# Kernel tuning notes

Hardware: AMD Instinct MI355X
Metric: run time of the kernel (lower is better)

The kernel has to match this reference:

```python
import jax, jax.numpy as jnp
import numpy as np
import math

B, S, D, H = 4, 1024, 2048, 16
DH = D // H          # dim_head = 128
DHID = 128           # dim_hid
DKER = 64            # dim_ker
EPS = 1e-6


def setup_inputs() -> dict:
    key = jax.random.key(0)
    ks = jax.random.split(key, 12)
    a1 = math.sqrt(6.0 / (DH + DHID))
    a2 = math.sqrt(6.0 / (DKER + DHID))
    a3 = math.sqrt(6.0 / (2 * DKER))
    return {
        "q": jax.random.normal(ks[0], (B, S, D), jnp.float32),
        "k": jax.random.normal(ks[1], (B, S, D), jnp.float32),
        "v": jax.random.normal(ks[2], (B, S, D), jnp.float32),
        "lr_attn_mask": jax.random.randint(ks[3], (B, 1, S, S), 0, 2).astype(bool),
        "sparse_norms_lse": jax.random.normal(ks[4], (B, H, S, 1), jnp.float32),
        "sparse_attn_weights": jax.random.normal(ks[5], (B, H, S, S), jnp.float32),
        "kernel_q_mat1": jax.random.uniform(ks[6], (H, DH, DHID), jnp.float32, -a1, a1),
        "kernel_k_mat1": jax.random.uniform(ks[7], (H, DH, DHID), jnp.float32, -a1, a1),
        "kernel_q_mat2": jax.random.uniform(ks[8], (H, DHID, DKER), jnp.float32, -a2, a2),
        "kernel_k_mat2": jax.random.uniform(ks[9], (H, DHID, DKER), jnp.float32, -a2, a2),
        "interaction_k": jax.random.uniform(ks[10], (H, DKER, DKER), jnp.float32, -a3, a3),
        "scalingD": jnp.ones((1, H, 1, DKER), jnp.float32) * 1e-4,
        "scalingD2": jnp.ones((1, H, 1, DKER), jnp.float32) * 1e-4,
        "lambda_constant": 1,
    }


def _gelu(x):
    # torch F.gelu default = exact (erf) gelu
    return jax.nn.gelu(x, approximate=False)


def reference(q, k, v, lr_attn_mask, sparse_norms_lse, sparse_attn_weights,
              kernel_q_mat1, kernel_k_mat1, kernel_q_mat2, kernel_k_mat2,
              interaction_k, scalingD, scalingD2, lambda_constant):
    # split heads: [B,S,D] -> [B,H,S,DH]
    qh = q.reshape(B, S, H, DH).transpose(0, 2, 1, 3)
    kh = k.reshape(B, S, H, DH).transpose(0, 2, 1, 3)
    vh = v.reshape(B, S, H, DH).transpose(0, 2, 1, 3)

    # learned kernel feature maps (dropout=0 -> identity)
    qf = _gelu(jnp.einsum('bhsd,hde->bhse', qh, kernel_q_mat1))
    qf = _gelu(jnp.einsum('bhse,hef->bhsf', qf, kernel_q_mat2))

    kf = _gelu(jnp.einsum('bhsd,hde->bhse', kh, kernel_k_mat1))
    kf = jnp.abs(scalingD) * _gelu(jnp.einsum('bhse,hef->bhsf', kf, kernel_k_mat2))
    kf = kf + jnp.einsum('bhse,hef->bhsf', kf, interaction_k) * scalingD2

    # low-rank (kernelized) scores, masked. [B,H,S,S]
    scores = jnp.einsum('bhse,bhte->bhst', jnp.abs(qf), jnp.abs(kf))
    m = lr_attn_mask.astype(scores.dtype)  # [B,1,S,S] broadcasts
    scores = m * scores

    # log-domain merge with external sparse attention
    lr_norms_lse = jnp.log(scores.sum(axis=-1, keepdims=True) + EPS)
    norm_factor_lse = jnp.logaddexp(lr_norms_lse, sparse_norms_lse)
    logits = jnp.log(scores + EPS) * m + (1.0 - m) * sparse_attn_weights
    attn = jnp.exp(logits - norm_factor_lse)

    out = jnp.einsum('bhst,bhtd->bhsd', attn, vh)
    return out.transpose(0, 2, 1, 3).reshape(B, S, D)
```

## Files before the change

kernel.cpp:

```cpp
#include <hip/hip_runtime.h>


typedef __bf16 bf16_t;
typedef __attribute__((ext_vector_type(8))) __bf16 bf16x8;
typedef __attribute__((ext_vector_type(4))) float f32x4;

#define MFMA(a, b, c) __builtin_amdgcn_mfma_f32_16x16x32_bf16((a), (b), (c), 0, 0, 0)

typedef __attribute__((address_space(3))) void as3_void;
typedef __attribute__((address_space(1))) const void as1_void;
static __device__ __forceinline__ void gload16(const void* g, void* l) {
    __builtin_amdgcn_global_load_lds((as1_void*)g, (as3_void*)l, 16, 0, 0);
}

static __device__ __forceinline__ float gelu_exact(float x) {
    return 0.5f * x * (1.0f + erff(x * 0.70710678118654752f));
}

static __device__ __forceinline__ unsigned pack_bf16(float a, float b) {
    bf16_t x = (bf16_t)a, y = (bf16_t)b;
    unsigned short ux = __builtin_bit_cast(unsigned short, x);
    unsigned short uy = __builtin_bit_cast(unsigned short, y);
    return (unsigned)ux | ((unsigned)uy << 16);
}

__global__ __launch_bounds__(256) void conv_weights_kernel(
    const float* __restrict__ wq1, const float* __restrict__ wk1,
    const float* __restrict__ wq2, const float* __restrict__ wk2,
    const float* __restrict__ iK,
    bf16_t* __restrict__ wq1t, bf16_t* __restrict__ wk1t,
    bf16_t* __restrict__ wq2t, bf16_t* __restrict__ wk2t,
    bf16_t* __restrict__ iKt)
{
    const int idx = blockIdx.x * 256 + threadIdx.x;
    if (idx < 16 * 128 * 128) {
        int h = idx >> 14, e = (idx >> 7) & 127, d = idx & 127;
        wq1t[idx] = (bf16_t)wq1[(h << 14) + (d << 7) + e];
        wk1t[idx] = (bf16_t)wk1[(h << 14) + (d << 7) + e];
    }
    if (idx < 16 * 64 * 128) {
        int h = idx >> 13, f = (idx >> 7) & 63, e = idx & 127;
        wq2t[idx] = (bf16_t)wq2[(h << 13) + (e << 6) + f];
        wk2t[idx] = (bf16_t)wk2[(h << 13) + (e << 6) + f];
    }
    if (idx < 16 * 64 * 64) {
        int h = idx >> 12, g = (idx >> 6) & 63, f = idx & 63;
        iKt[idx] = (bf16_t)iK[(h << 12) + (f << 6) + g];
    }
}

__global__ __launch_bounds__(256) void prep_kernel(
    const float* __restrict__ q, const float* __restrict__ k,
    const float* __restrict__ v, const unsigned char* __restrict__ mask8,
    const bf16_t* __restrict__ wq1t, const bf16_t* __restrict__ wq2t,
    const bf16_t* __restrict__ wk1t, const bf16_t* __restrict__ wk2t,
    const bf16_t* __restrict__ iKt,
    const float* __restrict__ sD, const float* __restrict__ sD2,
    bf16_t* __restrict__ qf, bf16_t* __restrict__ kf,
    bf16_t* __restrict__ vT, unsigned char* __restrict__ mprep)
{
    __shared__ char smem[44032];
    const int bxg = blockIdx.x;
    const int tid = threadIdx.x;

    if (bxg < 1024) {
        __shared__ int mflag;
        if (tid == 0) {
            unsigned a = 0;
            for (int i = 0; i < 64; ++i) a |= mask8[4 * i + 1];
            mflag = (a == 0) ? 1 : 0;
        }
        __syncthreads();
        const size_t base = ((size_t)bxg * 256 + tid) * 16;
        if (mflag) {
            const int* mi = (const int*)mask8;
            uint4 r;
            unsigned bs[4];
#pragma unroll
            for (int j = 0; j < 4; ++j) {
                int4 vv = *reinterpret_cast<const int4*>(&mi[base + j * 4]);
                bs[j] = (vv.x ? 1u : 0u) | ((vv.y ? 1u : 0u) << 8) |
                        ((vv.z ? 1u : 0u) << 16) | ((vv.w ? 1u : 0u) << 24);
            }
            r.x = bs[0]; r.y = bs[1]; r.z = bs[2]; r.w = bs[3];
            *reinterpret_cast<uint4*>(&mprep[base]) = r;
        } else {
            uint4 vv = *reinterpret_cast<const uint4*>(&mask8[base]);
            uint4 r;
            unsigned* pv = (unsigned*)&vv;
            unsigned* pr = (unsigned*)&r;
#pragma unroll
            for (int j = 0; j < 4; ++j) {
                unsigned x = pv[j], o = 0;
#pragma unroll
                for (int kk = 0; kk < 4; ++kk)
                    o |= (((x >> (8 * kk)) & 255u) ? 1u : 0u) << (8 * kk);
                pr[j] = o;
            }
            *reinterpret_cast<uint4*>(&mprep[base]) = r;
        }
        return;
    }

    if (bxg < 2048) {
        typedef bf16_t tr_t[72];
        tr_t* tr = reinterpret_cast<tr_t*>(smem);
        const int idv = bxg - 1024;
        const int bh = idv & 63, b = bh >> 4, h = bh & 15;
        const int tt = idv >> 6;
        const int t0 = tt * 64;
#pragma unroll
        for (int i = 0; i < 8; ++i) {
            int f4 = tid + 256 * i;
            int t = f4 >> 5, c4 = f4 & 31;
            const float4 vv = *reinterpret_cast<const float4*>(
                &v[((size_t)b * 1024 + t0 + t) * 2048 + h * 128 + c4 * 4]);
            tr[c4 * 4 + 0][t] = (bf16_t)vv.x;
            tr[c4 * 4 + 1][t] = (bf16_t)vv.y;
            tr[c4 * 4 + 2][t] = (bf16_t)vv.z;
            tr[c4 * 4 + 3][t] = (bf16_t)vv.w;
        }
        __syncthreads();
#pragma unroll
        for (int i = 0; i < 32; ++i) {
            int e = tid + 256 * i;
            int d = e >> 6, tl = e & 63;
            vT[(((size_t)bh * 16 + tt) * 128 + d) * 64 + tl] = tr[d][tl];
        }
        return;
    }

    {
        typedef bf16_t row136[136];
        typedef bf16_t row72[72];
        row136* xa = reinterpret_cast<row136*>(smem);
        row136* h1 = reinterpret_cast<row136*>(smem + 17408);
        row72*  k2 = reinterpret_cast<row72*>(smem + 34816);

        const int idf = bxg - 2048;
        const int lane = tid & 63, w = tid >> 6;
        const int lr = lane & 15, lg = lane >> 4;
        const int row0 = (idf & 63) * 64;
        const int h = (idf >> 6) & 15;
        const int path = idf >> 10;

        const float* X = path ? k : q;
        const bf16_t* w1t = path ? wk1t : wq1t;
        const bf16_t* w2t = path ? wk2t : wq2t;
        bf16_t* outp = path ? kf : qf;

#pragma unroll
        for (int i = 0; i < 8; ++i) {
            int f4 = tid + 256 * i;
            int r = f4 >> 5, c4 = f4 & 31;
            const float4 vv = *reinterpret_cast<const float4*>(
                &X[(size_t)(row0 + r) * 2048 + h * 128 + c4 * 4]);
            xa[r][c4 * 4 + 0] = (bf16_t)vv.x;
            xa[r][c4 * 4 + 1] = (bf16_t)vv.y;
            xa[r][c4 * 4 + 2] = (bf16_t)vv.z;
            xa[r][c4 * 4 + 3] = (bf16_t)vv.w;
        }
        __syncthreads();

        bf16x8 a1[4];
#pragma unroll
        for (int kk = 0; kk < 4; ++kk)
            a1[kk] = *reinterpret_cast<const bf16x8*>(&xa[w * 16 + lr][kk * 32 + lg * 8]);
#pragma unroll
        for (int nt = 0; nt < 8; ++nt) {
            f32x4 acc = {0.f, 0.f, 0.f, 0.f};
#pragma unroll
            for (int kk = 0; kk < 4; ++kk) {
                bf16x8 bfr = *reinterpret_cast<const bf16x8*>(
                    &w1t[(size_t)h * 16384 + (nt * 16 + lr) * 128 + kk * 32 + lg * 8]);
                acc = MFMA(a1[kk], bfr, acc);
            }
#pragma unroll
            for (int r = 0; r < 4; ++r)
                h1[w * 16 + lg * 4 + r][nt * 16 + lr] = (bf16_t)gelu_exact(acc[r]);
        }
        __syncthreads();

        bf16x8 a2[4];
#pragma unroll
        for (int kk = 0; kk < 4; ++kk)
            a2[kk] = *reinterpret_cast<const bf16x8*>(&h1[w * 16 + lr][kk * 32 + lg * 8]);

        if (path == 0) {
#pragma unroll
            for (int nt = 0; nt < 4; ++nt) {
                f32x4 acc = {0.f, 0.f, 0.f, 0.f};
#pragma unroll
                for (int kk = 0; kk < 4; ++kk) {
                    bf16x8 bfr = *reinterpret_cast<const bf16x8*>(
                        &w2t[(size_t)h * 8192 + (nt * 16 + lr) * 128 + kk * 32 + lg * 8]);
                    acc = MFMA(a2[kk], bfr, acc);
                }
#pragma unroll
                for (int r = 0; r < 4; ++r) {
                    int n = row0 + w * 16 + lg * 4 + r;
                    int bb = n >> 10, s = n & 1023;
                    outp[(((size_t)bb * 16 + h) * 1024 + s) * 64 + nt * 16 + lr] =
                        (bf16_t)fabsf(gelu_exact(acc[r]));
                }
            }
        } else {
#pragma unroll
            for (int nt = 0; nt < 4; ++nt) {
                f32x4 acc = {0.f, 0.f, 0.f, 0.f};
#pragma unroll
                for (int kk = 0; kk < 4; ++kk) {
                    bf16x8 bfr = *reinterpret_cast<const bf16x8*>(
                        &w2t[(size_t)h * 8192 + (nt * 16 + lr) * 128 + kk * 32 + lg * 8]);
                    acc = MFMA(a2[kk], bfr, acc);
                }
#pragma unroll
                for (int r = 0; r < 4; ++r) {
                    int f = nt * 16 + lr;
                    k2[w * 16 + lg * 4 + r][f] =
                        (bf16_t)(fabsf(sD[h * 64 + f]) * gelu_exact(acc[r]));
                }
            }
            __syncthreads();
            bf16x8 a3[2];
#pragma unroll
            for (int kk = 0; kk < 2; ++kk)
                a3[kk] = *reinterpret_cast<const bf16x8*>(&k2[w * 16 + lr][kk * 32 + lg * 8]);
#pragma unroll
            for (int nt = 0; nt < 4; ++nt) {
                f32x4 acc = {0.f, 0.f, 0.f, 0.f};
#pragma unroll
                for (int kk = 0; kk < 2; ++kk) {
                    bf16x8 bfr = *reinterpret_cast<const bf16x8*>(
                        &iKt[(size_t)h * 4096 + (nt * 16 + lr) * 64 + kk * 32 + lg * 8]);
                    acc = MFMA(a3[kk], bfr, acc);
                }
#pragma unroll
                for (int r = 0; r < 4; ++r) {
                    int row = w * 16 + lg * 4 + r;
                    int g = nt * 16 + lr;
                    float base = (float)k2[row][g];
                    float kv = fabsf(base + acc[r] * sD2[h * 64 + g]);
                    int n = row0 + row;
                    int bb = n >> 10, s = n & 1023;
                    outp[(((size_t)bb * 16 + h) * 1024 + s) * 64 + g] = (bf16_t)kv;
                }
            }
        }
    }
}

__global__ __launch_bounds__(256, 2) void attn_cv_kernel(
    const bf16_t* __restrict__ qf, const bf16_t* __restrict__ kf,
    const bf16_t* __restrict__ vT,
    const unsigned char* __restrict__ mprep,
    const float* __restrict__ saw, const float* __restrict__ lse,
    float* __restrict__ out)
{
    __shared__ bf16_t vbuf[3][128 * 64];
    __shared__ bf16_t kbuf[3][64 * 64];

    const int tid = threadIdx.x;
    const int lane = tid & 63, w = tid >> 6;
    const int lr = lane & 15, lg = lane >> 4;

    const int di = blockIdx.y * 16 + blockIdx.x;
    const int xcd = di & 7, rr = di >> 3;
    const int bh = xcd + 8 * (rr >> 4);
    const int s0 = (rr & 15) * 64;
    const int b = bh >> 4, h = bh & 15;

    const int srow = s0 + w * 16 + lr;
    const size_t saw_row = ((size_t)bh << 20) + (size_t)srow * 1024;
    const size_t m_row   = ((size_t)b << 20) + (size_t)srow * 1024;

    const int vrow = tid >> 3;
    const int vcol8 = (tid & 7) ^ (vrow & 7);
    const bf16_t* vt_bh = vT + (size_t)bh * 131072;
    const bf16_t* kf_bh = kf + (size_t)bh * 65536;

    bf16x8 aq0, aq1;
    {
        const size_t qb = ((size_t)bh * 1024 + srow) * 64;
        aq0 = *reinterpret_cast<const bf16x8*>(&qf[qb + lg * 8]);
        aq1 = *reinterpret_cast<const bf16x8*>(&qf[qb + 32 + lg * 8]);
    }

    const f32x4 fzero = {0.f, 0.f, 0.f, 0.f};
    f32x4 oacc[8];
#pragma unroll
    for (int i = 0; i < 8; ++i) oacc[i] = fzero;
    float rs = 0.f;

#define STAGE_VT(BUF, TILE)                                                      \
    {                                                                            \
        const bf16_t* vg = vt_bh + (size_t)(TILE) * 8192 + vcol8 * 8;            \
        char* lb = (char*)&vbuf[BUF][0] + w * 1024;                              \
        _Pragma("unroll")                                                        \
        for (int j = 0; j < 4; ++j)                                              \
            gload16(vg + (size_t)(32 * j + vrow) * 64, lb + j * 4096);           \
    }

#define STAGE_KF(BUF, TILE)                                                      \
    {                                                                            \
        const bf16_t* kg = kf_bh + (size_t)(TILE) * 4096 + vcol8 * 8;            \
        char* lb = (char*)&kbuf[BUF][0] + w * 1024;                              \
        _Pragma("unroll")                                                        \
        for (int j = 0; j < 2; ++j)                                              \
            gload16(kg + (size_t)(32 * j + vrow) * 64, lb + j * 4096);           \
    }

#define LOAD_SAW(TILE, SS, MM)                                                   \
    {                                                                            \
        _Pragma("unroll")                                                        \
        for (int nt = 0; nt < 4; ++nt) {                                         \
            SS[nt] = *reinterpret_cast<const f32x4*>(                            \
                &saw[saw_row + (size_t)(TILE) * 64 + nt * 16 + lg * 4]);         \
            MM[nt] = *reinterpret_cast<const unsigned*>(                         \
                &mprep[m_row + (size_t)(TILE) * 64 + nt * 16 + lg * 4]);         \
        }                                                                        \
    }

#define QKT_MERGE(CUR, SS, MM)                                                   \
    {                                                                            \
        _Pragma("unroll")                                                        \
        for (int nt = 0; nt < 4; ++nt) {                                         \
            const int row = nt * 16 + lr;                                        \
            const char* kb = (const char*)&kbuf[CUR][0] + row * 128;             \
            const int sw = (row & 7) * 16;                                       \
            bf16x8 k0 = *reinterpret_cast<const bf16x8*>(kb + ((lg * 16) ^ sw)); \
            bf16x8 k1 = *reinterpret_cast<const bf16x8*>(kb + ((64 + lg * 16) ^ sw)); \
            f32x4 acc = fzero;                                                   \
            acc = MFMA(k0, aq0, acc);                                            \
            acc = MFMA(k1, aq1, acc);                                            \
            const unsigned mm = MM[nt];                                          \
            float v0, v1, v2, v3;                                                \
            v0 = (mm & 255u)         ? (acc[0] + 1e-6f) : __expf(SS[nt][0]);     \
            rs += (mm & 255u)         ? acc[0] : 0.f;                            \
            v1 = ((mm >> 8) & 255u)  ? (acc[1] + 1e-6f) : __expf(SS[nt][1]);     \
            rs += ((mm >> 8) & 255u)  ? acc[1] : 0.f;                            \
            v2 = ((mm >> 16) & 255u) ? (acc[2] + 1e-6f) : __expf(SS[nt][2]);     \
            rs += ((mm >> 16) & 255u) ? acc[2] : 0.f;                            \
            v3 = (mm >> 24)          ? (acc[3] + 1e-6f) : __expf(SS[nt][3]);     \
            rs += (mm >> 24)          ? acc[3] : 0.f;                            \
            pk[nt * 2]     = pack_bf16(v0, v1);                                  \
            pk[nt * 2 + 1] = pack_bf16(v2, v3);                                  \
        }                                                                        \
    }

#define REDIST()                                                                 \
    {                                                                            \
        const int srcA = lr + ((lg & 1) << 5);                                   \
        const int srcB = srcA + 16;                                              \
        const bool sel = (lg < 2);                                               \
        const unsigned a0 = __shfl(pk[0], srcA, 64);                             \
        const unsigned a1 = __shfl(pk[1], srcA, 64);                             \
        const unsigned a2 = __shfl(pk[2], srcA, 64);                             \
        const unsigned a3 = __shfl(pk[3], srcA, 64);                             \
        const unsigned b0 = __shfl(pk[0], srcB, 64);                             \
        const unsigned b1 = __shfl(pk[1], srcB, 64);                             \
        const unsigned b2 = __shfl(pk[2], srcB, 64);                             \
        const unsigned b3 = __shfl(pk[3], srcB, 64);                             \
        f0w.x = sel ? a0 : a2;  f0w.y = sel ? a1 : a3;                           \
        f0w.z = sel ? b0 : b2;  f0w.w = sel ? b1 : b3;                           \
        const unsigned c4 = __shfl(pk[4], srcA, 64);                             \
        const unsigned c5 = __shfl(pk[5], srcA, 64);                             \
        const unsigned c6 = __shfl(pk[6], srcA, 64);                             \
        const unsigned c7 = __shfl(pk[7], srcA, 64);                             \
        const unsigned d4 = __shfl(pk[4], srcB, 64);                             \
        const unsigned d5 = __shfl(pk[5], srcB, 64);                             \
        const unsigned d6 = __shfl(pk[6], srcB, 64);                             \
        const unsigned d7 = __shfl(pk[7], srcB, 64);                             \
        f1w.x = sel ? c4 : c6;  f1w.y = sel ? c5 : c7;                           \
        f1w.z = sel ? d4 : d6;  f1w.w = sel ? d5 : d7;                           \
    }

#define PV(CUR)                                                                  \
    {                                                                            \
        bf16x8 pf0 = __builtin_bit_cast(bf16x8, f0w);                            \
        bf16x8 pf1 = __builtin_bit_cast(bf16x8, f1w);                            \
        __builtin_amdgcn_s_setprio(1);                                           \
        _Pragma("unroll")                                                        \
        for (int dt = 0; dt < 8; ++dt) {                                         \
            const int row = dt * 16 + lr;                                        \
            const char* vb = (const char*)&vbuf[CUR][0] + row * 128;             \
            const int sw = (row & 7) * 16;                                       \
            bf16x8 v0 = *reinterpret_cast<const bf16x8*>(vb + ((lg * 16) ^ sw)); \
            bf16x8 v1 = *reinterpret_cast<const bf16x8*>(vb + ((64 + lg * 16) ^ sw)); \
            oacc[dt] = MFMA(v0, pf0, oacc[dt]);                                  \
            oacc[dt] = MFMA(v1, pf1, oacc[dt]);                                  \
        }                                                                        \
        __builtin_amdgcn_s_setprio(0);                                           \
    }

#define FULL_PHASE(CIDX, SIDX, TSTAGE, SS, MM, TSAW)                             \
    {                                                                            \
        STAGE_VT(SIDX, TSTAGE);                                                  \
        STAGE_KF(SIDX, TSTAGE);                                                  \
        __builtin_amdgcn_sched_barrier(0);                                       \
        asm volatile("s_waitcnt vmcnt(28)" ::: "memory");                        \
        __builtin_amdgcn_s_barrier();                                            \
        __builtin_amdgcn_sched_barrier(0);                                       \
        QKT_MERGE(CIDX, SS, MM);                                                 \
        REDIST();                                                                \
        LOAD_SAW(TSAW, SS, MM);                                                  \
        __builtin_amdgcn_sched_barrier(0);                                       \
        PV(CIDX);                                                                \
        __builtin_amdgcn_sched_barrier(0);                                       \
        __builtin_amdgcn_s_barrier();                                            \
    }

    f32x4 sawA[4], sawB[4];
    unsigned muA[4], muB[4];
    unsigned pk[8];
    uint4 f0w, f1w;

    STAGE_VT(0, 0);
    STAGE_KF(0, 0);
    LOAD_SAW(0, sawA, muA);
    STAGE_VT(1, 1);
    STAGE_KF(1, 1);
    LOAD_SAW(1, sawB, muB);

    int c0 = 0, c1 = 1, c2 = 2;
    for (int i = 0; i < 14; i += 2) {
        FULL_PHASE(c0, c2, i + 2, sawA, muA, i + 2);
        FULL_PHASE(c1, c0, i + 3, sawB, muB, i + 3);
        const int t_ = c0; c0 = c2; c2 = c1; c1 = t_;
    }

    {
        asm volatile("s_waitcnt vmcnt(22)" ::: "memory");
        __builtin_amdgcn_s_barrier();
        __builtin_amdgcn_sched_barrier(0);
        QKT_MERGE(c0, sawA, muA);
        REDIST();
        __builtin_amdgcn_sched_barrier(0);
        PV(c0);
        __builtin_amdgcn_sched_barrier(0);
        __builtin_amdgcn_s_barrier();
    }
    {
        asm volatile("s_waitcnt vmcnt(8)" ::: "memory");
        __builtin_amdgcn_s_barrier();
        __builtin_amdgcn_sched_barrier(0);
        QKT_MERGE(c1, sawB, muB);
        REDIST();
        __builtin_amdgcn_sched_barrier(0);
        PV(c1);
    }

    rs += __shfl_xor(rs, 16);
    rs += __shfl_xor(rs, 32);
    const float invden =
        1.0f / (rs + 1e-6f + __expf(lse[(size_t)bh * 1024 + srow]));

    const size_t ob = ((size_t)b * 1024 + srow) * 2048 + h * 128 + lg * 4;
#pragma unroll
    for (int dt = 0; dt < 8; ++dt) {
        f32x4 o;
        o[0] = oacc[dt][0] * invden;
        o[1] = oacc[dt][1] * invden;
        o[2] = oacc[dt][2] * invden;
        o[3] = oacc[dt][3] * invden;
        *reinterpret_cast<f32x4*>(&out[ob + dt * 16]) = o;
    }
#undef STAGE_VT
#undef STAGE_KF
#undef LOAD_SAW
#undef QKT_MERGE
#undef REDIST
#undef PV
#undef FULL_PHASE
}

extern "C" void kernel_launch(void* const* d_in, const int* in_sizes, int n_in,
                              void* d_out, int out_size, void* d_ws, size_t ws_size,
                              hipStream_t stream)
{
    const float* q   = (const float*)d_in[0];
    const float* k   = (const float*)d_in[1];
    const float* v   = (const float*)d_in[2];
    const unsigned char* mask = (const unsigned char*)d_in[3];
    const float* lse = (const float*)d_in[4];
    const float* saw = (const float*)d_in[5];
    const float* wq1 = (const float*)d_in[6];
    const float* wk1 = (const float*)d_in[7];
    const float* wq2 = (const float*)d_in[8];
    const float* wk2 = (const float*)d_in[9];
    const float* iK  = (const float*)d_in[10];
    const float* sD  = (const float*)d_in[11];
    const float* sD2 = (const float*)d_in[12];
    float* out = (float*)d_out;

    bf16_t* wsb  = (bf16_t*)d_ws;
    bf16_t* wq1t = wsb;
    bf16_t* wk1t = wq1t + 262144;
    bf16_t* wq2t = wk1t + 262144;
    bf16_t* wk2t = wq2t + 131072;
    bf16_t* iKt  = wk2t + 131072;
    bf16_t* qf   = iKt  + 65536;
    bf16_t* kf   = qf   + 4194304;
    bf16_t* vT   = kf   + 4194304;
    unsigned char* mprep = (unsigned char*)(vT + 8388608);

    conv_weights_kernel<<<dim3(1024), dim3(256), 0, stream>>>(
        wq1, wk1, wq2, wk2, iK, wq1t, wk1t, wq2t, wk2t, iKt);
    prep_kernel<<<dim3(4096), dim3(256), 0, stream>>>(
        q, k, v, mask, wq1t, wq2t, wk1t, wk2t, iKt, sD, sD2, qf, kf, vT, mprep);
    attn_cv_kernel<<<dim3(16, 64), dim3(256), 0, stream>>>(
        qf, kf, vT, mprep, saw, lse, out);
}
```

Before: 188.2 us.

## Stage sparse weights through LDS and load key features directly into registers

Sparse attention weights are now copied with async global-to-LDS loads into a double-buffered, XOR-swizzled shared tile. Key features, which were previously staged in LDS, are now loaded straight into registers one tile ahead. The pipeline's waitcnt depths and prologue/epilogue are rebalanced to match. The aim is to make the large fp32 sparse-weight stream coalesced and asynchronous rather than per-lane register loads. In exchange, register pressure and LDS use (now 2x16KB fp32) go up, which could hurt occupancy.

```diff
diff --git a/kernel.cpp b/kernel.cpp
--- a/kernel.cpp
+++ b/kernel.cpp
@@ -258,7 +258,7 @@
     float* __restrict__ out)
 {
     __shared__ bf16_t vbuf[3][128 * 64];
-    __shared__ bf16_t kbuf[3][64 * 64];
+    __shared__ float  sawbuf[2][64 * 64];
 
     const int tid = threadIdx.x;
     const int lane = tid & 63, w = tid >> 6;
@@ -271,13 +271,16 @@
     const int b = bh >> 4, h = bh & 15;
 
     const int srow = s0 + w * 16 + lr;
-    const size_t saw_row = ((size_t)bh << 20) + (size_t)srow * 1024;
-    const size_t m_row   = ((size_t)b << 20) + (size_t)srow * 1024;
+    const size_t m_row = ((size_t)b << 20) + (size_t)srow * 1024;
 
     const int vrow = tid >> 3;
     const int vcol8 = (tid & 7) ^ (vrow & 7);
     const bf16_t* vt_bh = vT + (size_t)bh * 131072;
     const bf16_t* kf_bh = kf + (size_t)bh * 65536;
+
+    const int s_subrow = lane >> 4;
+    const int s_cc = lane & 15;
+    const float* saw_bh = saw + ((size_t)bh << 20);
 
     bf16x8 aq0, aq1;
     {
@@ -301,47 +304,56 @@
             gload16(vg + (size_t)(32 * j + vrow) * 64, lb + j * 4096);           \
     }
 
-#define STAGE_KF(BUF, TILE)                                                      \
-    {                                                                            \
-        const bf16_t* kg = kf_bh + (size_t)(TILE) * 4096 + vcol8 * 8;            \
-        char* lb = (char*)&kbuf[BUF][0] + w * 1024;                              \
+#define STAGE_SAW(SB, TILE)                                                      \
+    {                                                                            \
         _Pragma("unroll")                                                        \
-        for (int j = 0; j < 2; ++j)                                              \
-            gload16(kg + (size_t)(32 * j + vrow) * 64, lb + j * 4096);           \
-    }
-
-#define LOAD_SAW(TILE, SS, MM)                                                   \
+        for (int j = 0; j < 4; ++j) {                                            \
+            const int row_ = j * 16 + w * 4 + s_subrow;                          \
+            const float* sg = saw_bh + (size_t)(s0 + row_) * 1024                \
+                            + (size_t)(TILE) * 64 + ((s_cc ^ (row_ & 15)) << 2); \
+            char* lb = (char*)&sawbuf[SB][0] + j * 4096 + w * 1024;              \
+            gload16(sg, lb);                                                     \
+        }                                                                        \
+    }
+
+#define LOAD_KF(TILE, KR)                                                        \
     {                                                                            \
         _Pragma("unroll")                                                        \
         for (int nt = 0; nt < 4; ++nt) {                                         \
-            SS[nt] = *reinterpret_cast<const f32x4*>(                            \
-                &saw[saw_row + (size_t)(TILE) * 64 + nt * 16 + lg * 4]);         \
+            const size_t kb = ((size_t)(TILE) * 64 + nt * 16 + lr) * 64;         \
+            KR[nt * 2]     = *reinterpret_cast<const bf16x8*>(&kf_bh[kb + lg * 8]); \
+            KR[nt * 2 + 1] = *reinterpret_cast<const bf16x8*>(&kf_bh[kb + 32 + lg * 8]); \
+        }                                                                        \
+    }
+
+#define LOAD_MASK(TILE, MM)                                                      \
+    {                                                                            \
+        _Pragma("unroll")                                                        \
+        for (int nt = 0; nt < 4; ++nt)                                           \
             MM[nt] = *reinterpret_cast<const unsigned*>(                         \
                 &mprep[m_row + (size_t)(TILE) * 64 + nt * 16 + lg * 4]);         \
-        }                                                                        \
-    }
-
-#define QKT_MERGE(CUR, SS, MM)                                                   \
-    {                                                                            \
+    }
+
+#define QKT_MERGE(SB, KR, MM)                                                    \
+    {                                                                            \
+        const int lrow_ = w * 16 + lr;                                           \
+        const float* sb_ = &sawbuf[SB][0] + lrow_ * 64;                          \
         _Pragma("unroll")                                                        \
         for (int nt = 0; nt < 4; ++nt) {                                         \
-            const int row = nt * 16 + lr;                                        \
-            const char* kb = (const char*)&kbuf[CUR][0] + row * 128;             \
-            const int sw = (row & 7) * 16;                                       \
-            bf16x8 k0 = *reinterpret_cast<const bf16x8*>(kb + ((lg * 16) ^ sw)); \
-            bf16x8 k1 = *reinterpret_cast<const bf16x8*>(kb + ((64 + lg * 16) ^ sw)); \
             f32x4 acc = fzero;                                                   \
-            acc = MFMA(k0, aq0, acc);                                            \
-            acc = MFMA(k1, aq1, acc);                                            \
+            acc = MFMA(KR[nt * 2], aq0, acc);                                    \
+            acc = MFMA(KR[nt * 2 + 1], aq1, acc);                                \
+            const f32x4 sv = *reinterpret_cast<const f32x4*>(                    \
+                sb_ + (((nt * 4 + lg) ^ lr) << 2));                              \
             const unsigned mm = MM[nt];                                          \
             float v0, v1, v2, v3;                                                \
-            v0 = (mm & 255u)         ? (acc[0] + 1e-6f) : __expf(SS[nt][0]);     \
+            v0 = (mm & 255u)         ? (acc[0] + 1e-6f) : __expf(sv[0]);         \
             rs += (mm & 255u)         ? acc[0] : 0.f;                            \
-            v1 = ((mm >> 8) & 255u)  ? (acc[1] + 1e-6f) : __expf(SS[nt][1]);     \
+            v1 = ((mm >> 8) & 255u)  ? (acc[1] + 1e-6f) : __expf(sv[1]);         \
             rs += ((mm >> 8) & 255u)  ? acc[1] : 0.f;                            \
-            v2 = ((mm >> 16) & 255u) ? (acc[2] + 1e-6f) : __expf(SS[nt][2]);     \
+            v2 = ((mm >> 16) & 255u) ? (acc[2] + 1e-6f) : __expf(sv[2]);         \
             rs += ((mm >> 16) & 255u) ? acc[2] : 0.f;                            \
-            v3 = (mm >> 24)          ? (acc[3] + 1e-6f) : __expf(SS[nt][3]);     \
+            v3 = (mm >> 24)          ? (acc[3] + 1e-6f) : __expf(sv[3]);         \
             rs += (mm >> 24)          ? acc[3] : 0.f;                            \
             pk[nt * 2]     = pack_bf16(v0, v1);                                  \
             pk[nt * 2 + 1] = pack_bf16(v2, v3);                                  \
@@ -393,47 +405,51 @@
         __builtin_amdgcn_s_setprio(0);                                           \
     }
 
-#define FULL_PHASE(CIDX, SIDX, TSTAGE, SS, MM, TSAW)                             \
-    {                                                                            \
-        STAGE_VT(SIDX, TSTAGE);                                                  \
-        STAGE_KF(SIDX, TSTAGE);                                                  \
+#define FULL_PHASE(CIDX, SIDX, I, SBC, KRC, MMC, KRN, MMN)                       \
+    {                                                                            \
+        STAGE_VT(SIDX, (I) + 2);                                                 \
+        STAGE_SAW(((I) + 1) & 1, (I) + 1);                                       \
+        LOAD_KF((I) + 1, KRN);                                                   \
+        LOAD_MASK((I) + 1, MMN);                                                 \
         __builtin_amdgcn_sched_barrier(0);                                       \
-        asm volatile("s_waitcnt vmcnt(28)" ::: "memory");                        \
+        asm volatile("s_waitcnt vmcnt(32)" ::: "memory");                        \
         __builtin_amdgcn_s_barrier();                                            \
         __builtin_amdgcn_sched_barrier(0);                                       \
-        QKT_MERGE(CIDX, SS, MM);                                                 \
+        QKT_MERGE(SBC, KRC, MMC);                                                \
         REDIST();                                                                \
-        LOAD_SAW(TSAW, SS, MM);                                                  \
         __builtin_amdgcn_sched_barrier(0);                                       \
         PV(CIDX);                                                                \
         __builtin_amdgcn_sched_barrier(0);                                       \
         __builtin_amdgcn_s_barrier();                                            \
     }
 
-    f32x4 sawA[4], sawB[4];
     unsigned muA[4], muB[4];
+    bf16x8 kfA[8], kfB[8];
     unsigned pk[8];
     uint4 f0w, f1w;
 
     STAGE_VT(0, 0);
-    STAGE_KF(0, 0);
-    LOAD_SAW(0, sawA, muA);
     STAGE_VT(1, 1);
-    STAGE_KF(1, 1);
-    LOAD_SAW(1, sawB, muB);
+    STAGE_SAW(0, 0);
+    LOAD_KF(0, kfA);
+    LOAD_MASK(0, muA);
 
     int c0 = 0, c1 = 1, c2 = 2;
     for (int i = 0; i < 14; i += 2) {
-        FULL_PHASE(c0, c2, i + 2, sawA, muA, i + 2);
-        FULL_PHASE(c1, c0, i + 3, sawB, muB, i + 3);
+        FULL_PHASE(c0, c2, i,     (i & 1),       kfA, muA, kfB, muB);
+        FULL_PHASE(c1, c0, i + 1, ((i + 1) & 1), kfB, muB, kfA, muA);
         const int t_ = c0; c0 = c2; c2 = c1; c1 = t_;
     }
 
     {
-        asm volatile("s_waitcnt vmcnt(22)" ::: "memory");
+        STAGE_SAW(1, 15);
+        LOAD_KF(15, kfB);
+        LOAD_MASK(15, muB);
+        __builtin_amdgcn_sched_barrier(0);
+        asm volatile("s_waitcnt vmcnt(28)" ::: "memory");
         __builtin_amdgcn_s_barrier();
         __builtin_amdgcn_sched_barrier(0);
-        QKT_MERGE(c0, sawA, muA);
+        QKT_MERGE(0, kfA, muA);
         REDIST();
         __builtin_amdgcn_sched_barrier(0);
         PV(c0);
@@ -441,10 +457,10 @@
         __builtin_amdgcn_s_barrier();
     }
     {
-        asm volatile("s_waitcnt vmcnt(8)" ::: "memory");
+        asm volatile("s_waitcnt vmcnt(12)" ::: "memory");
         __builtin_amdgcn_s_barrier();
         __builtin_amdgcn_sched_barrier(0);
-        QKT_MERGE(c1, sawB, muB);
+        QKT_MERGE(1, kfB, muB);
         REDIST();
         __builtin_amdgcn_sched_barrier(0);
         PV(c1);
@@ -466,8 +482,9 @@
         *reinterpret_cast<f32x4*>(&out[ob + dt * 16]) = o;
     }
 #undef STAGE_VT
-#undef STAGE_KF
-#undef LOAD_SAW
+#undef STAGE_SAW
+#undef LOAD_KF
+#undef LOAD_MASK
 #undef QKT_MERGE
 #undef REDIST
 #undef PV
```

New measurement: 230.3 us. 1.22x slower.

## Load key features directly into registers and raise occupancy to three blocks

Applied to the files above, without the earlier changes.

Removes the triple-buffered LDS staging of the kernelized key tile and instead loads key-feature fragments straight from global memory into registers, one tile ahead, alongside the saw/mask prefetch. This frees LDS and raises the launch bound to three blocks per CU to improve latency hiding. It also reworks the pipeline so K and saw for tile i+1 are issued at the start of each phase, with vmcnt waits adjusted to match. The trade-off is more register pressure from 16 extra bf16x8 fragments under a tighter register budget, possible spills, and K loads that are now less coalesced and duplicated across waves.

```diff
diff --git a/kernel.cpp b/kernel.cpp
--- a/kernel.cpp
+++ b/kernel.cpp
@@ -250,7 +250,7 @@
     }
 }
 
-__global__ __launch_bounds__(256, 2) void attn_cv_kernel(
+__global__ __launch_bounds__(256, 3) void attn_cv_kernel(
     const bf16_t* __restrict__ qf, const bf16_t* __restrict__ kf,
     const bf16_t* __restrict__ vT,
     const unsigned char* __restrict__ mprep,
@@ -258,7 +258,6 @@
     float* __restrict__ out)
 {
     __shared__ bf16_t vbuf[3][128 * 64];
-    __shared__ bf16_t kbuf[3][64 * 64];
 
     const int tid = threadIdx.x;
     const int lane = tid & 63, w = tid >> 6;
@@ -292,6 +291,7 @@
     for (int i = 0; i < 8; ++i) oacc[i] = fzero;
     float rs = 0.f;
 
+
 #define STAGE_VT(BUF, TILE)                                                      \
     {                                                                            \
         const bf16_t* vg = vt_bh + (size_t)(TILE) * 8192 + vcol8 * 8;            \
@@ -301,13 +301,14 @@
             gload16(vg + (size_t)(32 * j + vrow) * 64, lb + j * 4096);           \
     }
 
-#define STAGE_KF(BUF, TILE)                                                      \
-    {                                                                            \
-        const bf16_t* kg = kf_bh + (size_t)(TILE) * 4096 + vcol8 * 8;            \
-        char* lb = (char*)&kbuf[BUF][0] + w * 1024;                              \
+#define LOAD_KF(TILE, KR)                                                        \
+    {                                                                            \
         _Pragma("unroll")                                                        \
-        for (int j = 0; j < 2; ++j)                                              \
-            gload16(kg + (size_t)(32 * j + vrow) * 64, lb + j * 4096);           \
+        for (int nt = 0; nt < 4; ++nt) {                                         \
+            const size_t kb = ((size_t)(TILE) * 64 + nt * 16 + lr) * 64;         \
+            KR[nt * 2]     = *reinterpret_cast<const bf16x8*>(&kf_bh[kb + lg * 8]); \
+            KR[nt * 2 + 1] = *reinterpret_cast<const bf16x8*>(&kf_bh[kb + 32 + lg * 8]); \
+        }                                                                        \
     }
 
 #define LOAD_SAW(TILE, SS, MM)                                                   \
@@ -321,18 +322,13 @@
         }                                                                        \
     }
 
-#define QKT_MERGE(CUR, SS, MM)                                                   \
+#define QKT_MERGE(KR, SS, MM)                                                    \
     {                                                                            \
         _Pragma("unroll")                                                        \
         for (int nt = 0; nt < 4; ++nt) {                                         \
-            const int row = nt * 16 + lr;                                        \
-            const char* kb = (const char*)&kbuf[CUR][0] + row * 128;             \
-            const int sw = (row & 7) * 16;                                       \
-            bf16x8 k0 = *reinterpret_cast<const bf16x8*>(kb + ((lg * 16) ^ sw)); \
-            bf16x8 k1 = *reinterpret_cast<const bf16x8*>(kb + ((64 + lg * 16) ^ sw)); \
             f32x4 acc = fzero;                                                   \
-            acc = MFMA(k0, aq0, acc);                                            \
-            acc = MFMA(k1, aq1, acc);                                            \
+            acc = MFMA(KR[nt * 2], aq0, acc);                                    \
+            acc = MFMA(KR[nt * 2 + 1], aq1, acc);                                \
             const unsigned mm = MM[nt];                                          \
             float v0, v1, v2, v3;                                                \
             v0 = (mm & 255u)         ? (acc[0] + 1e-6f) : __expf(SS[nt][0]);     \
@@ -393,17 +389,17 @@
         __builtin_amdgcn_s_setprio(0);                                           \
     }
 
-#define FULL_PHASE(CIDX, SIDX, TSTAGE, SS, MM, TSAW)                             \
-    {                                                                            \
-        STAGE_VT(SIDX, TSTAGE);                                                  \
-        STAGE_KF(SIDX, TSTAGE);                                                  \
+#define FULL_PHASE(CIDX, SIDX, I, KRC, SSC, MMC, KRN, SSN, MMN)                  \
+    {                                                                            \
+        LOAD_KF((I) + 1, KRN);                                                   \
+        LOAD_SAW((I) + 1, SSN, MMN);                                             \
+        STAGE_VT(SIDX, (I) + 2);                                                 \
         __builtin_amdgcn_sched_barrier(0);                                       \
-        asm volatile("s_waitcnt vmcnt(28)" ::: "memory");                        \
+        asm volatile("s_waitcnt vmcnt(24)" ::: "memory");                        \
         __builtin_amdgcn_s_barrier();                                            \
         __builtin_amdgcn_sched_barrier(0);                                       \
-        QKT_MERGE(CIDX, SS, MM);                                                 \
+        QKT_MERGE(KRC, SSC, MMC);                                                \
         REDIST();                                                                \
-        LOAD_SAW(TSAW, SS, MM);                                                  \
         __builtin_amdgcn_sched_barrier(0);                                       \
         PV(CIDX);                                                                \
         __builtin_amdgcn_sched_barrier(0);                                       \
@@ -412,28 +408,30 @@
 
     f32x4 sawA[4], sawB[4];
     unsigned muA[4], muB[4];
+    bf16x8 kfA[8], kfB[8];
     unsigned pk[8];
     uint4 f0w, f1w;
 
+    LOAD_KF(0, kfA);
+    LOAD_SAW(0, sawA, muA);
     STAGE_VT(0, 0);
-    STAGE_KF(0, 0);
-    LOAD_SAW(0, sawA, muA);
     STAGE_VT(1, 1);
-    STAGE_KF(1, 1);
-    LOAD_SAW(1, sawB, muB);
 
     int c0 = 0, c1 = 1, c2 = 2;
     for (int i = 0; i < 14; i += 2) {
-        FULL_PHASE(c0, c2, i + 2, sawA, muA, i + 2);
-        FULL_PHASE(c1, c0, i + 3, sawB, muB, i + 3);
+        FULL_PHASE(c0, c2, i,     kfA, sawA, muA, kfB, sawB, muB);
+        FULL_PHASE(c1, c0, i + 1, kfB, sawB, muB, kfA, sawA, muA);
         const int t_ = c0; c0 = c2; c2 = c1; c1 = t_;
     }
 
     {
-        asm volatile("s_waitcnt vmcnt(22)" ::: "memory");
+        LOAD_KF(15, kfB);
+        LOAD_SAW(15, sawB, muB);
+        __builtin_amdgcn_sched_barrier(0);
+        asm volatile("s_waitcnt vmcnt(20)" ::: "memory");
         __builtin_amdgcn_s_barrier();
         __builtin_amdgcn_sched_barrier(0);
-        QKT_MERGE(c0, sawA, muA);
+        QKT_MERGE(kfA, sawA, muA);
         REDIST();
         __builtin_amdgcn_sched_barrier(0);
         PV(c0);
@@ -441,10 +439,10 @@
         __builtin_amdgcn_s_barrier();
     }
     {
-        asm volatile("s_waitcnt vmcnt(8)" ::: "memory");
+        asm volatile("s_waitcnt vmcnt(0)" ::: "memory");
         __builtin_amdgcn_s_barrier();
         __builtin_amdgcn_sched_barrier(0);
-        QKT_MERGE(c1, sawB, muB);
+        QKT_MERGE(kfB, sawB, muB);
         REDIST();
         __builtin_amdgcn_sched_barrier(0);
         PV(c1);
@@ -466,7 +464,7 @@
         *reinterpret_cast<f32x4*>(&out[ob + dt * 16]) = o;
     }
 #undef STAGE_VT
-#undef STAGE_KF
+#undef LOAD_KF
 #undef LOAD_SAW
 #undef QKT_MERGE
 #undef REDIST
```

After: 232.6 us. 23.6% more time.
